# Kernel optimization log

Measured on AMD Instinct MI355X. Metric: run time of the kernel, lower is better.

## Reference

```python
import jax, jax.numpy as jnp
import numpy as np

EMB = 16
N_LEFT = 200000
N_RIGHT = 200000
N_EDGES = 4000000


def _linear_params(key, out_dim, in_dim, bias=True):
    k1, k2 = jax.random.split(key)
    bound = 1.0 / np.sqrt(in_dim)
    W = jax.random.uniform(k1, (out_dim, in_dim), minval=-bound, maxval=bound, dtype=jnp.float32)
    if bias:
        b = jax.random.uniform(k2, (out_dim,), minval=-bound, maxval=bound, dtype=jnp.float32)
        return W, b
    return W


def setup_inputs() -> dict:
    key = jax.random.key(0)
    ks = jax.random.split(key, 12)
    left_features = jax.random.normal(ks[0], (N_LEFT, EMB), dtype=jnp.float32)
    right_features = jax.random.normal(ks[1], (N_RIGHT, EMB), dtype=jnp.float32)
    edge_features = jax.random.normal(ks[2], (N_EDGES, 1), dtype=jnp.float32)
    left_idx = jax.random.randint(ks[3], (N_EDGES,), 0, N_LEFT)
    right_idx = jax.random.randint(ks[4], (N_EDGES,), 0, N_RIGHT)
    edge_indices = jnp.stack([left_idx, right_idx], axis=0).astype(jnp.int64)

    W_left, b_left = _linear_params(ks[5], EMB, EMB, bias=True)
    W_edge = _linear_params(ks[6], EMB, 1, bias=False)
    W_right = _linear_params(ks[7], EMB, EMB, bias=False)
    W_final, b_final = _linear_params(ks[8], EMB, EMB, bias=True)
    W_post, b_post = _linear_params(ks[9], EMB, EMB, bias=True)
    W_out1, b_out1 = _linear_params(ks[10], EMB, 2 * EMB, bias=True)
    W_out2, b_out2 = _linear_params(ks[11], EMB, EMB, bias=True)

    return {
        "left_features": left_features,
        "edge_features": edge_features,
        "right_features": right_features,
        "edge_indices": edge_indices,
        "W_left": W_left, "b_left": b_left,
        "W_edge": W_edge,
        "W_right": W_right,
        "W_final": W_final, "b_final": b_final,
        "W_post": W_post, "b_post": b_post,
        "W_out1": W_out1, "b_out1": b_out1,
        "W_out2": W_out2, "b_out2": b_out2,
    }


def reference(left_features, edge_features, right_features, edge_indices,
              W_left, b_left, W_edge, W_right, W_final, b_final,
              W_post, b_post, W_out1, b_out1, W_out2, b_out2):
    n_right = right_features.shape[0]
    left_idx = edge_indices[0]
    right_idx = edge_indices[1]

    # per-edge message: Linear(left gathered) + edge Linear + Linear(right gathered)
    pre = (left_features[left_idx] @ W_left.T + b_left
           + edge_features @ W_edge.T
           + right_features[right_idx] @ W_right.T)  # [E, emb]
    msg = jax.nn.relu(pre) @ W_final.T + b_final     # fm_final: ReLU -> Linear

    # scatter-add aggregate per right node
    aggregated = jax.ops.segment_sum(msg, right_idx, num_segments=n_right)  # [n_right, emb]

    post = jax.nn.relu(aggregated) @ W_post.T + b_post  # post: ReLU -> Linear
    cat = jnp.concatenate([post, right_features], axis=-1)  # [n_right, 2*emb]
    h = jax.nn.relu(cat @ W_out1.T + b_out1)
    return h @ W_out2.T + b_out2
```

## Files before the change

### kernel.cpp

```cpp
#include <hip/hip_runtime.h>
#include <hip/hip_bf16.h>
#include <hip/hip_fp16.h>

#define EMB 16
#define EPT 4

typedef _Float16 half8 __attribute__((ext_vector_type(8)));

__global__ __launch_bounds__(256) void node_transform2_kernel(
    const float* __restrict__ left, const float* __restrict__ right,
    const float* __restrict__ Wl, const float* __restrict__ bl,
    const float* __restrict__ Wr,
    _Float16* __restrict__ TL, _Float16* __restrict__ TR, int NL, int NR) {
    __shared__ float sWl[EMB * EMB], sWr[EMB * EMB], sbl[EMB];
    if (threadIdx.x < EMB * EMB) {
        sWl[threadIdx.x] = Wl[threadIdx.x];
        sWr[threadIdx.x] = Wr[threadIdx.x];
    }
    if (threadIdx.x < EMB) sbl[threadIdx.x] = bl[threadIdx.x];
    __syncthreads();

    int n = blockIdx.x * blockDim.x + threadIdx.x;
    if (n >= NL + NR) return;
    bool is_left = (n < NL);
    const float* X = is_left ? (left + (size_t)n * EMB)
                             : (right + (size_t)(n - NL) * EMB);
    _Float16* Y = is_left ? (TL + (size_t)n * EMB)
                          : (TR + (size_t)(n - NL) * EMB);
    const float* sW = is_left ? sWl : sWr;

    float x[EMB];
    const float4* xp = (const float4*)X;
    float4 x0 = xp[0], x1 = xp[1], x2 = xp[2], x3 = xp[3];
    x[0] = x0.x; x[1] = x0.y; x[2] = x0.z; x[3] = x0.w;
    x[4] = x1.x; x[5] = x1.y; x[6] = x1.z; x[7] = x1.w;
    x[8] = x2.x; x[9] = x2.y; x[10] = x2.z; x[11] = x2.w;
    x[12] = x3.x; x[13] = x3.y; x[14] = x3.z; x[15] = x3.w;

    float y[EMB];
#pragma unroll
    for (int j = 0; j < EMB; ++j) {
        float a = is_left ? sbl[j] : 0.0f;
#pragma unroll
        for (int k = 0; k < EMB; ++k) a = fmaf(sW[j * EMB + k], x[k], a);
        y[j] = a;
    }

    half8* yp = (half8*)Y;
    half8 h0, h1;
#pragma unroll
    for (int k = 0; k < 8; ++k) h0[k] = (_Float16)y[k];
#pragma unroll
    for (int k = 0; k < 8; ++k) h1[k] = (_Float16)y[8 + k];
    yp[0] = h0;
    yp[1] = h1;
}

__global__ __launch_bounds__(256) void edge_scatter_kernel(
    const int* __restrict__ idx, const float* __restrict__ ef,
    const _Float16* __restrict__ TL, const _Float16* __restrict__ TR,
    const float* __restrict__ wedge, const float* __restrict__ Wf,
    const float* __restrict__ bf, __half2* __restrict__ S, int E, int G) {
    int gid = blockIdx.x * blockDim.x + threadIdx.x;
    int g = gid >> 4;
    int t = gid & 15;

    int lane = threadIdx.x & 63;
    int gbase = lane & 48;
    int bp0 = (gbase | ((2 * t) & 15)) << 2;
    int bp1 = (gbase | ((2 * t + 1) & 15)) << 2;

    float we = wedge[t];
    float bft = bf[t];
    float wrow[EMB];
    {
        const float4* wp = (const float4*)(Wf + t * EMB);
        float4 w0 = wp[0], w1 = wp[1], w2 = wp[2], w3 = wp[3];
        wrow[0] = w0.x; wrow[1] = w0.y; wrow[2] = w0.z; wrow[3] = w0.w;
        wrow[4] = w1.x; wrow[5] = w1.y; wrow[6] = w1.z; wrow[7] = w1.w;
        wrow[8] = w2.x; wrow[9] = w2.y; wrow[10] = w2.z; wrow[11] = w2.w;
        wrow[12] = w3.x; wrow[13] = w3.y; wrow[14] = w3.z; wrow[15] = w3.w;
    }

    int l[EPT], r[EPT];
    float efv[EPT];
    bool valid[EPT];
#pragma unroll
    for (int j = 0; j < EPT; ++j) {
        int e = g + j * G;
        valid[j] = (e < E);
        int ec = valid[j] ? e : 0;
        l[j] = idx[ec];
        r[j] = idx[E + ec];
        efv[j] = ef[ec];
    }

    _Float16 ah[EPT], bh[EPT];
#pragma unroll
    for (int j = 0; j < EPT; ++j) {
        ah[j] = TL[(size_t)l[j] * EMB + t];
        bh[j] = TR[(size_t)r[j] * EMB + t];
    }

#pragma unroll
    for (int j = 0; j < EPT; ++j) {
        float v = fmaxf((float)ah[j] + (float)bh[j] + efv[j] * we, 0.0f);
        int vi = __float_as_int(v);
        float w = bft;
#define SWIZ_STEP(K)                                                          \
        {                                                                     \
            float vk = __int_as_float(                                        \
                __builtin_amdgcn_ds_swizzle(vi, ((K) << 5) | 0x10));          \
            w = fmaf(wrow[K], vk, w);                                         \
        }
        SWIZ_STEP(0)  SWIZ_STEP(1)  SWIZ_STEP(2)  SWIZ_STEP(3)
        SWIZ_STEP(4)  SWIZ_STEP(5)  SWIZ_STEP(6)  SWIZ_STEP(7)
        SWIZ_STEP(8)  SWIZ_STEP(9)  SWIZ_STEP(10) SWIZ_STEP(11)
        SWIZ_STEP(12) SWIZ_STEP(13) SWIZ_STEP(14) SWIZ_STEP(15)
#undef SWIZ_STEP

        int wi = __float_as_int(w);
        float w0 = __int_as_float(__builtin_amdgcn_ds_bpermute(bp0, wi));
        float w1 = __int_as_float(__builtin_amdgcn_ds_bpermute(bp1, wi));
        if (valid[j] && t < 8) {
            __half2 hv = __floats2half2_rn(w0, w1);
            unsafeAtomicAdd(S + (size_t)r[j] * 8 + t, hv);
        }
    }
}

__global__ __launch_bounds__(256) void epilogue_kernel(
    const _Float16* __restrict__ S, const float* __restrict__ right,
    const float* __restrict__ Wp, const float* __restrict__ bp,
    const float* __restrict__ Wo1, const float* __restrict__ bo1,
    const float* __restrict__ Wo2, const float* __restrict__ bo2,
    float* __restrict__ out, int N) {
    __shared__ float sWp[256], sWo2[256], sWo1[512];
    __shared__ float sbp[16], sbo1[16], sbo2[16];
    for (int i = threadIdx.x; i < 256; i += blockDim.x) {
        sWp[i] = Wp[i]; sWo2[i] = Wo2[i];
    }
    for (int i = threadIdx.x; i < 512; i += blockDim.x) sWo1[i] = Wo1[i];
    if (threadIdx.x < 16) {
        sbp[threadIdx.x] = bp[threadIdx.x];
        sbo1[threadIdx.x] = bo1[threadIdx.x];
        sbo2[threadIdx.x] = bo2[threadIdx.x];
    }
    __syncthreads();

    int n = blockIdx.x * blockDim.x + threadIdx.x;
    if (n >= N) return;

    float ra[EMB];
    {
        const half8* sp = (const half8*)(S + (size_t)n * EMB);
        half8 a0 = sp[0], a1 = sp[1];
#pragma unroll
        for (int k = 0; k < 8; ++k) ra[k] = fmaxf((float)a0[k], 0.0f);
#pragma unroll
        for (int k = 0; k < 8; ++k) ra[8 + k] = fmaxf((float)a1[k], 0.0f);
    }

    float p[EMB];
#pragma unroll
    for (int j = 0; j < EMB; ++j) {
        float a = sbp[j];
#pragma unroll
        for (int k = 0; k < EMB; ++k) a = fmaf(sWp[j * EMB + k], ra[k], a);
        p[j] = a;
    }

    float rf[EMB];
    {
        const float4* rp = (const float4*)(right + (size_t)n * EMB);
        float4 a0 = rp[0], a1 = rp[1], a2 = rp[2], a3 = rp[3];
        rf[0] = a0.x; rf[1] = a0.y; rf[2] = a0.z; rf[3] = a0.w;
        rf[4] = a1.x; rf[5] = a1.y; rf[6] = a1.z; rf[7] = a1.w;
        rf[8] = a2.x; rf[9] = a2.y; rf[10] = a2.z; rf[11] = a2.w;
        rf[12] = a3.x; rf[13] = a3.y; rf[14] = a3.z; rf[15] = a3.w;
    }

    float h[EMB];
#pragma unroll
    for (int j = 0; j < EMB; ++j) {
        float a = sbo1[j];
#pragma unroll
        for (int k = 0; k < EMB; ++k) a = fmaf(sWo1[j * 32 + k], p[k], a);
#pragma unroll
        for (int k = 0; k < EMB; ++k) a = fmaf(sWo1[j * 32 + 16 + k], rf[k], a);
        h[j] = fmaxf(a, 0.0f);
    }

    float o[EMB];
#pragma unroll
    for (int j = 0; j < EMB; ++j) {
        float a = sbo2[j];
#pragma unroll
        for (int k = 0; k < EMB; ++k) a = fmaf(sWo2[j * EMB + k], h[k], a);
        o[j] = a;
    }

    float4* op = (float4*)(out + (size_t)n * EMB);
    op[0] = make_float4(o[0], o[1], o[2], o[3]);
    op[1] = make_float4(o[4], o[5], o[6], o[7]);
    op[2] = make_float4(o[8], o[9], o[10], o[11]);
    op[3] = make_float4(o[12], o[13], o[14], o[15]);
}

extern "C" void kernel_launch(void* const* d_in, const int* in_sizes, int n_in,
                              void* d_out, int out_size, void* d_ws, size_t ws_size,
                              hipStream_t stream) {
    const float* left  = (const float*)d_in[0];
    const float* ef    = (const float*)d_in[1];
    const float* right = (const float*)d_in[2];
    const int*   eidx  = (const int*)d_in[3];
    const float* W_left  = (const float*)d_in[4];
    const float* b_left  = (const float*)d_in[5];
    const float* W_edge  = (const float*)d_in[6];
    const float* W_right = (const float*)d_in[7];
    const float* W_final = (const float*)d_in[8];
    const float* b_final = (const float*)d_in[9];
    const float* W_post  = (const float*)d_in[10];
    const float* b_post  = (const float*)d_in[11];
    const float* W_out1  = (const float*)d_in[12];
    const float* b_out1  = (const float*)d_in[13];
    const float* W_out2  = (const float*)d_in[14];
    const float* b_out2  = (const float*)d_in[15];

    const int NL = in_sizes[0] / EMB;
    const int NR = in_sizes[2] / EMB;
    const int E  = in_sizes[1];

    size_t tl_b = (size_t)NL * EMB * 2;
    size_t tr_b = (size_t)NR * EMB * 2;
    char* ws = (char*)d_ws;
    _Float16* TL = (_Float16*)ws;
    _Float16* TR = (_Float16*)(ws + tl_b);
    _Float16* S16 = (_Float16*)(ws + tl_b + tr_b);

    (void)hipMemsetAsync(S16, 0, (size_t)NR * EMB * 2, stream);

    node_transform2_kernel<<<(NL + NR + 255) / 256, 256, 0, stream>>>(
        left, right, W_left, b_left, W_right, TL, TR, NL, NR);

    {
        int G = (E + EPT - 1) / EPT;
        long long threads = (long long)G * 16;
        int blocks = (int)((threads + 255) / 256);
        edge_scatter_kernel<<<blocks, 256, 0, stream>>>(
            eidx, ef, TL, TR, W_edge, W_final, b_final, (__half2*)S16, E, G);
    }

    epilogue_kernel<<<(NR + 255) / 256, 256, 0, stream>>>(
        S16, right, W_post, b_post, W_out1, b_out1, W_out2, b_out2,
        (float*)d_out, NR);
}
```

Measured before the change: 354.2 us.

## Bin edges by destination bucket and aggregate in LDS with MFMA

```diff
diff --git a/kernel.cpp b/kernel.cpp
--- a/kernel.cpp
+++ b/kernel.cpp
@@ -3,9 +3,15 @@
 #include <hip/hip_fp16.h>
 
 #define EMB 16
-#define EPT 4
+#define BN 128
+#define BKT_SHIFT 7
+#define MAXBKT 1600
+#define CAP 3072
+#define B3_CHUNK 4096
+#define CUR_STRIDE 16
 
 typedef _Float16 half8 __attribute__((ext_vector_type(8)));
+typedef float f32x4 __attribute__((ext_vector_type(4)));
 
 __global__ __launch_bounds__(256) void node_transform2_kernel(
     const float* __restrict__ left, const float* __restrict__ right,
@@ -56,76 +62,170 @@
     yp[1] = h1;
 }
 
-__global__ __launch_bounds__(256) void edge_scatter_kernel(
+__global__ __launch_bounds__(256) void bin_kernel(
     const int* __restrict__ idx, const float* __restrict__ ef,
+    unsigned* __restrict__ cursor, uint2* __restrict__ rec, int E, int nbkt) {
+    __shared__ unsigned s_off[MAXBKT];
+    __shared__ unsigned s_gb[MAXBKT];
+    __shared__ unsigned s_scan[256];
+    __shared__ uint2 s_stage[B3_CHUNK];
+    __shared__ unsigned s_dst[B3_CHUNK];
+
+    const int tid = threadIdx.x;
+    const int base = blockIdx.x * B3_CHUNK;
+    const int nval = min(B3_CHUNK, E - base);
+
+    for (int i = tid; i < nbkt; i += 256) s_off[i] = 0u;
+    __syncthreads();
+
+    unsigned w0v[16];
+    float efv[16];
+    int bkv[16];
+#pragma unroll
+    for (int j = 0; j < 16; ++j) {
+        int e = base + tid + j * 256;
+        bool v = (e < E);
+        int ec = v ? e : 0;
+        int l = idx[ec];
+        int r = idx[E + ec];
+        efv[j] = ef[ec];
+        bkv[j] = v ? (r >> BKT_SHIFT) : -1;
+        w0v[j] = (unsigned)l | ((unsigned)(r & (BN - 1)) << 20);
+        if (v) atomicAdd(&s_off[bkv[j]], 1u);
+    }
+    __syncthreads();
+
+    unsigned loc[7];
+    unsigned run = 0;
+#pragma unroll
+    for (int k = 0; k < 7; ++k) {
+        int i = tid * 7 + k;
+        unsigned v = (i < nbkt) ? s_off[i] : 0u;
+        loc[k] = run;
+        run += v;
+    }
+    s_scan[tid] = run;
+    __syncthreads();
+    for (int off = 1; off < 256; off <<= 1) {
+        unsigned add = (tid >= off) ? s_scan[tid - off] : 0u;
+        __syncthreads();
+        s_scan[tid] += add;
+        __syncthreads();
+    }
+    unsigned ex = (tid == 0) ? 0u : s_scan[tid - 1];
+#pragma unroll
+    for (int k = 0; k < 7; ++k) {
+        int i = tid * 7 + k;
+        if (i < nbkt) {
+            unsigned c = s_off[i];
+            s_off[i] = ex + loc[k];
+            s_gb[i] = c;
+        }
+    }
+    __syncthreads();
+
+    for (int i = tid; i < nbkt; i += 256) {
+        unsigned c = s_gb[i];
+        if (c) {
+            unsigned g = atomicAdd(&cursor[(size_t)i * CUR_STRIDE], c);
+            s_gb[i] = (unsigned)i * CAP + g - s_off[i];
+        }
+    }
+    __syncthreads();
+
+#pragma unroll
+    for (int j = 0; j < 16; ++j) {
+        if (bkv[j] >= 0) {
+            unsigned p = atomicAdd(&s_off[bkv[j]], 1u);
+            s_stage[p] = make_uint2(w0v[j], __float_as_uint(efv[j]));
+            s_dst[p] = s_gb[bkv[j]] + p;
+        }
+    }
+    __syncthreads();
+
+    for (int p = tid; p < nval; p += 256) rec[s_dst[p]] = s_stage[p];
+}
+
+__global__ __launch_bounds__(256) void bucket_process_kernel(
+    const uint2* __restrict__ rec, const unsigned* __restrict__ cursor,
     const _Float16* __restrict__ TL, const _Float16* __restrict__ TR,
     const float* __restrict__ wedge, const float* __restrict__ Wf,
-    const float* __restrict__ bf, __half2* __restrict__ S, int E, int G) {
-    int gid = blockIdx.x * blockDim.x + threadIdx.x;
-    int g = gid >> 4;
-    int t = gid & 15;
-
-    int lane = threadIdx.x & 63;
-    int gbase = lane & 48;
-    int bp0 = (gbase | ((2 * t) & 15)) << 2;
-    int bp1 = (gbase | ((2 * t + 1) & 15)) << 2;
-
-    float we = wedge[t];
-    float bft = bf[t];
-    float wrow[EMB];
+    const float* __restrict__ bf, _Float16* __restrict__ S, int NR, int nbkt) {
+    __shared__ __align__(16) float sAcc[(BN + 1) * EMB];
+    __shared__ __align__(16) _Float16 sTR[(BN + 1) * EMB];
+
+    const int tid = threadIdx.x;
+    const int b = blockIdx.x;
+    const int node0 = b * BN;
+    const int nrow = min(BN, NR - node0);
+
+    for (int i = tid; i < (BN + 1) * EMB; i += 256) sAcc[i] = 0.0f;
     {
-        const float4* wp = (const float4*)(Wf + t * EMB);
-        float4 w0 = wp[0], w1 = wp[1], w2 = wp[2], w3 = wp[3];
-        wrow[0] = w0.x; wrow[1] = w0.y; wrow[2] = w0.z; wrow[3] = w0.w;
-        wrow[4] = w1.x; wrow[5] = w1.y; wrow[6] = w1.z; wrow[7] = w1.w;
-        wrow[8] = w2.x; wrow[9] = w2.y; wrow[10] = w2.z; wrow[11] = w2.w;
-        wrow[12] = w3.x; wrow[13] = w3.y; wrow[14] = w3.z; wrow[15] = w3.w;
-    }
-
-    int l[EPT], r[EPT];
-    float efv[EPT];
-    bool valid[EPT];
-#pragma unroll
-    for (int j = 0; j < EPT; ++j) {
-        int e = g + j * G;
-        valid[j] = (e < E);
-        int ec = valid[j] ? e : 0;
-        l[j] = idx[ec];
-        r[j] = idx[E + ec];
-        efv[j] = ef[ec];
-    }
-
-    _Float16 ah[EPT], bh[EPT];
-#pragma unroll
-    for (int j = 0; j < EPT; ++j) {
-        ah[j] = TL[(size_t)l[j] * EMB + t];
-        bh[j] = TR[(size_t)r[j] * EMB + t];
-    }
-
-#pragma unroll
-    for (int j = 0; j < EPT; ++j) {
-        float v = fmaxf((float)ah[j] + (float)bh[j] + efv[j] * we, 0.0f);
-        int vi = __float_as_int(v);
-        float w = bft;
-#define SWIZ_STEP(K)                                                          \
-        {                                                                     \
-            float vk = __int_as_float(                                        \
-                __builtin_amdgcn_ds_swizzle(vi, ((K) << 5) | 0x10));          \
-            w = fmaf(wrow[K], vk, w);                                         \
-        }
-        SWIZ_STEP(0)  SWIZ_STEP(1)  SWIZ_STEP(2)  SWIZ_STEP(3)
-        SWIZ_STEP(4)  SWIZ_STEP(5)  SWIZ_STEP(6)  SWIZ_STEP(7)
-        SWIZ_STEP(8)  SWIZ_STEP(9)  SWIZ_STEP(10) SWIZ_STEP(11)
-        SWIZ_STEP(12) SWIZ_STEP(13) SWIZ_STEP(14) SWIZ_STEP(15)
-#undef SWIZ_STEP
-
-        int wi = __float_as_int(w);
-        float w0 = __int_as_float(__builtin_amdgcn_ds_bpermute(bp0, wi));
-        float w1 = __int_as_float(__builtin_amdgcn_ds_bpermute(bp1, wi));
-        if (valid[j] && t < 8) {
-            __half2 hv = __floats2half2_rn(w0, w1);
-            unsafeAtomicAdd(S + (size_t)r[j] * 8 + t, hv);
-        }
+        const uint4* src = (const uint4*)(TR + (size_t)node0 * EMB);
+        uint4* dst = (uint4*)sTR;
+        for (int i = tid; i < (BN + 1) * 2; i += 256)
+            dst[i] = (i < nrow * 2) ? src[i] : make_uint4(0u, 0u, 0u, 0u);
+    }
+    __syncthreads();
+
+    const int lane = tid & 63;
+    const int wid = tid >> 6;
+    const int m = lane & 15;
+    const int bb = lane >> 4;
+    const bool act = (bb < 2);
+
+    half8 bfrag, wev;
+#pragma unroll
+    for (int j = 0; j < 8; ++j) {
+        bfrag[j] = act ? (_Float16)Wf[m * EMB + bb * 8 + j] : (_Float16)0.0f;
+        wev[j]   = act ? (_Float16)wedge[bb * 8 + j] : (_Float16)0.0f;
+    }
+    const float bfn = bf[m];
+
+    const unsigned cnt = cursor[(size_t)b * CUR_STRIDE];
+    const uint2* recp = rec + (size_t)b * CAP;
+
+    for (unsigned eo = (unsigned)wid * 16u; eo < cnt; eo += 64u) {
+        unsigned ai = eo + (unsigned)m;
+        uint2 ra = recp[ai < cnt ? ai : 0u];
+        if (ai >= cnt) { ra.x = ((unsigned)BN) << 20; ra.y = 0u; }
+        unsigned lidx = ra.x & 0xFFFFFu;
+        unsigned rla = ra.x >> 20;
+        _Float16 feh = (_Float16)__uint_as_float(ra.y);
+
+        half8 afrag;
+        if (act) {
+            half8 ta = *(const half8*)(TL + (size_t)lidx * EMB + bb * 8);
+            half8 tb = *(const half8*)(sTR + (size_t)rla * EMB + bb * 8);
+            half8 pre = ta + tb + wev * feh;
+#pragma unroll
+            for (int j = 0; j < 8; ++j)
+                pre[j] = pre[j] > (_Float16)0.0f ? pre[j] : (_Float16)0.0f;
+            afrag = pre;
+        } else {
+#pragma unroll
+            for (int j = 0; j < 8; ++j) afrag[j] = (_Float16)0.0f;
+        }
+
+        f32x4 c = {bfn, bfn, bfn, bfn};
+        f32x4 d = __builtin_amdgcn_mfma_f32_16x16x32_f16(afrag, bfrag, c, 0, 0, 0);
+
+#pragma unroll
+        for (int r = 0; r < 4; ++r) {
+            unsigned si = eo + (unsigned)(bb * 4 + r);
+            uint2 rr = recp[si < cnt ? si : 0u];
+            unsigned rl2 = (si < cnt) ? (rr.x >> 20) : (unsigned)BN;
+            atomicAdd(&sAcc[rl2 * EMB + m], d[r]);
+        }
+    }
+    __syncthreads();
+
+    _Float16* out = S + (size_t)node0 * EMB;
+    for (int i = tid; i < nrow * 2; i += 256) {
+        half8 h;
+#pragma unroll
+        for (int j = 0; j < 8; ++j) h[j] = (_Float16)sAcc[i * 8 + j];
+        ((half8*)out)[i] = h;
     }
 }
 
@@ -230,26 +330,30 @@
     const int NL = in_sizes[0] / EMB;
     const int NR = in_sizes[2] / EMB;
     const int E  = in_sizes[1];
-
-    size_t tl_b = (size_t)NL * EMB * 2;
-    size_t tr_b = (size_t)NR * EMB * 2;
+    const int nbkt = (NR + BN - 1) / BN;
+
+    size_t tl_b  = (size_t)NL * EMB * 2;
+    size_t tr_b  = (size_t)NR * EMB * 2;
+    size_t s_b   = (size_t)NR * EMB * 2;
+    size_t cur_b = ((size_t)nbkt * CUR_STRIDE * 4 + 255) & ~(size_t)255;
+
     char* ws = (char*)d_ws;
-    _Float16* TL = (_Float16*)ws;
-    _Float16* TR = (_Float16*)(ws + tl_b);
-    _Float16* S16 = (_Float16*)(ws + tl_b + tr_b);
-
-    (void)hipMemsetAsync(S16, 0, (size_t)NR * EMB * 2, stream);
+    _Float16* TL   = (_Float16*)ws;
+    _Float16* TR   = (_Float16*)(ws + tl_b);
+    _Float16* S16  = (_Float16*)(ws + tl_b + tr_b);
+    unsigned* cursor = (unsigned*)(ws + tl_b + tr_b + s_b);
+    uint2*    rec    = (uint2*)(ws + tl_b + tr_b + s_b + cur_b);
+
+    (void)hipMemsetAsync(cursor, 0, (size_t)nbkt * CUR_STRIDE * 4, stream);
 
     node_transform2_kernel<<<(NL + NR + 255) / 256, 256, 0, stream>>>(
         left, right, W_left, b_left, W_right, TL, TR, NL, NR);
 
-    {
-        int G = (E + EPT - 1) / EPT;
-        long long threads = (long long)G * 16;
-        int blocks = (int)((threads + 255) / 256);
-        edge_scatter_kernel<<<blocks, 256, 0, stream>>>(
-            eidx, ef, TL, TR, W_edge, W_final, b_final, (__half2*)S16, E, G);
-    }
+    bin_kernel<<<(E + B3_CHUNK - 1) / B3_CHUNK, 256, 0, stream>>>(
+        eidx, ef, cursor, rec, E, nbkt);
+
+    bucket_process_kernel<<<nbkt, 256, 0, stream>>>(
+        rec, cursor, TL, TR, W_edge, W_final, b_final, S16, NR, nbkt);
 
     epilogue_kernel<<<(NR + 255) / 256, 256, 0, stream>>>(
         S16, right, W_post, b_post, W_out1, b_out1, W_out2, b_out2,
```

Result: slower. 637.2 us (+79.9%).
